# Optimization experiments

Hardware: AMD Instinct MI355X
Metric: run time of the kernel (lower is better)

The kernel has to match this reference:

```python
import jax, jax.numpy as jnp
import numpy as np

N_AUTHOR, N_PAPER = 20000, 40000
E = 400000
IN_DIM, HIDDEN, HEADS, NUM_CLASSES, NUM_LAYERS = 128, 128, 8, 16, 2
DIM = HIDDEN // HEADS
NEG_SLOPE = 0.2
AUTHOR_RAW = 64


def setup_inputs() -> dict:
    key = jax.random.key(0)
    ks = jax.random.split(key, 16)
    s = 0.05
    return {
        'x_author': jax.random.normal(ks[0], (N_AUTHOR, AUTHOR_RAW), jnp.float32),
        'x_paper': jax.random.normal(ks[1], (N_PAPER, IN_DIM), jnp.float32),
        'Wa': jax.random.normal(ks[2], (AUTHOR_RAW, IN_DIM), jnp.float32) * s,
        'proj_w': jax.random.normal(ks[3], (NUM_LAYERS, 2, IN_DIM, HIDDEN), jnp.float32) * s,
        'proj_b': jnp.zeros((NUM_LAYERS, 2, HIDDEN), jnp.float32),
        'att_src': jax.random.normal(ks[4], (NUM_LAYERS, 3, HEADS, DIM), jnp.float32) * s,
        'att_dst': jax.random.normal(ks[5], (NUM_LAYERS, 3, HEADS, DIM), jnp.float32) * s,
        'klin_w': jax.random.normal(ks[6], (NUM_LAYERS, HIDDEN, HIDDEN), jnp.float32) * s,
        'klin_b': jnp.zeros((NUM_LAYERS, HIDDEN), jnp.float32),
        'q': jax.random.normal(ks[7], (NUM_LAYERS, HIDDEN), jnp.float32) * s,
        'lin_w': jax.random.normal(ks[8], (HIDDEN, NUM_CLASSES), jnp.float32) * s,
        'lin_b': jnp.zeros((NUM_CLASSES,), jnp.float32),
        'ei_writes': jnp.stack([jax.random.randint(ks[9], (E,), 0, N_AUTHOR),
                                jax.random.randint(ks[10], (E,), 0, N_PAPER)]),
        'ei_written_by': jnp.stack([jax.random.randint(ks[11], (E,), 0, N_PAPER),
                                    jax.random.randint(ks[12], (E,), 0, N_AUTHOR)]),
        'ei_cites': jnp.stack([jax.random.randint(ks[13], (E,), 0, N_PAPER),
                               jax.random.randint(ks[14], (E,), 0, N_PAPER)]),
    }


def _segment_softmax(scores, seg, num_segments):
    # scores: [E, H]; softmax over edges sharing a destination node.
    m = jax.ops.segment_max(scores, seg, num_segments=num_segments)
    m = jnp.where(jnp.isfinite(m), m, 0.0)
    e = jnp.exp(scores - m[seg])
    denom = jax.ops.segment_sum(e, seg, num_segments=num_segments)
    return e / (denom[seg] + 1e-16)


def _han_forward(x_author, x_paper, Wa, proj_w, proj_b, att_src, att_dst,
                 klin_w, klin_b, q, lin_w, lin_b,
                 ei_writes, ei_written_by, ei_cites):
    # Type-alignment projector (author: 64 -> 128, no bias; paper: Identity)
    x = {'author': x_author @ Wa, 'paper': x_paper}
    nsize = {'author': N_AUTHOR, 'paper': N_PAPER}
    ntidx = {'author': 0, 'paper': 1}
    edge_types = [('author', 'paper', ei_writes),
                  ('paper', 'author', ei_written_by),
                  ('paper', 'paper', ei_cites)]
    for l in range(NUM_LAYERS):
        # Per-node-type projection -> [N, H, D]
        xh = {nt: (x[nt] @ proj_w[l, ntidx[nt]] + proj_b[l, ntidx[nt]]).reshape(-1, HEADS, DIM)
              for nt in x}
        outs = {'author': [], 'paper': []}
        for e_id, (src, dst, ei) in enumerate(edge_types):
            a_src = (xh[src] * att_src[l, e_id]).sum(-1)  # [N_src, H]
            a_dst = (xh[dst] * att_dst[l, e_id]).sum(-1)  # [N_dst, H]
            si, di = ei[0], ei[1]
            alpha = a_src[si] + a_dst[di]                 # [E, H]
            alpha = jnp.where(alpha >= 0, alpha, NEG_SLOPE * alpha)  # leaky_relu
            alpha = _segment_softmax(alpha, di, nsize[dst])
            # attention dropout omitted (eval mode)
            msg = (xh[src][si] * alpha[:, :, None]).reshape(-1, HIDDEN)  # [E, HIDDEN]
            agg = jax.ops.segment_sum(msg, di, num_segments=nsize[dst])
            outs[dst].append(jax.nn.relu(agg))
        # Semantic-level attention over metapath embeddings per node type
        newx = {}
        for nt, xs in outs.items():
            stk = jnp.stack(xs)  # [M, N, F]
            score = (q[l] * jnp.tanh(stk @ klin_w[l] + klin_b[l]).mean(axis=1)).sum(-1)  # [M]
            attn = jax.nn.softmax(score)
            newx[nt] = (attn[:, None, None] * stk).sum(0)
        x = newx
        if l < NUM_LAYERS - 1:
            x = {nt: jax.nn.relu(v) for nt, v in x.items()}
            # feature dropout omitted (eval mode)
    return x['paper'] @ lin_w + lin_b  # [N_PAPER, NUM_CLASSES]


def reference(x_author, x_paper, Wa, proj_w, proj_b, att_src, att_dst,
              klin_w, klin_b, q, lin_w, lin_b,
              ei_writes, ei_written_by, ei_cites):
    return _han_forward(x_author, x_paper, Wa, proj_w, proj_b, att_src, att_dst,
                        klin_w, klin_b, q, lin_w, lin_b,
                        ei_writes, ei_written_by, ei_cites)
```

## Files before the change

### kernel.cpp

```cpp
#include <hip/hip_runtime.h>
#include <hip/hip_bf16.h>

typedef __hip_bfloat16 bf16;
typedef __hip_bfloat162 bf162;

#define N_AUTHOR 20000
#define N_PAPER  40000
#define NEDGE    400000
#define HID      128
#define HEADS    8
#define DIMH     16
#define NCLS     16

typedef short short4v __attribute__((ext_vector_type(4)));
typedef short short8v __attribute__((ext_vector_type(8)));
typedef float f32x4   __attribute__((ext_vector_type(4)));

__device__ __forceinline__ bf162 mk2(float a, float b){
    bf162 r; r.x = __float2bfloat16(a); r.y = __float2bfloat16(b); return r;
}
__device__ __forceinline__ float b2f(short s){
    return __uint_as_float(((unsigned)(unsigned short)s) << 16);
}
__device__ __forceinline__ short f2bs(float v){
    unsigned u = __float_as_uint(v);
    unsigned r = (u + 0x7FFFu + ((u >> 16) & 1u)) >> 16;
    return (short)r;
}
__device__ __forceinline__ float fastrcp(float x){ return __builtin_amdgcn_rcpf(x); }

__device__ __forceinline__ float fast_tanh(float x){
    x = fminf(fmaxf(x, -15.f), 15.f);
    float e = __expf(2.f * x);
    return 1.f - 2.f * fastrcp(e + 1.f);
}

template<int KDIM, int EPI>
__device__ __forceinline__ void bgemm_body(
    const bf16* __restrict__ A, const bf16* __restrict__ Wt, const float* __restrict__ Bb,
    bf16* __restrict__ C, const float* __restrict__ qv, float* __restrict__ score,
    int M, int brow, float* red)
{
    const int tid  = threadIdx.x;
    const int lane = tid & 63;
    const int wv   = tid >> 6;
    const int lr   = lane & 15;
    const int quad = lane >> 4;
    const int row0 = brow * 64 + wv * 16;
    const int arow_i = row0 + lr;
    const bool rowok = arow_i < M;
    const bf16* arow = A + (long)arow_i * KDIM;

    short8v afrag[KDIM / 32];
    #pragma unroll
    for (int kc = 0; kc < KDIM / 32; kc++) {
        short8v f = {0,0,0,0,0,0,0,0};
        if (rowok) f = *(const short8v*)(arow + kc * 32 + quad * 8);
        afrag[kc] = f;
    }

    f32x4 acc[8];
    #pragma unroll
    for (int ct = 0; ct < 8; ct++) acc[ct] = (f32x4){0.f, 0.f, 0.f, 0.f};

    #pragma unroll
    for (int kc = 0; kc < KDIM / 32; kc++) {
        short8v bfrag[8];
        #pragma unroll
        for (int ct = 0; ct < 8; ct++)
            bfrag[ct] = *(const short8v*)(Wt + (long)(ct * 16 + lr) * KDIM + kc * 32 + quad * 8);
        #pragma unroll
        for (int ct = 0; ct < 8; ct++)
            acc[ct] = __builtin_amdgcn_mfma_f32_16x16x32_bf16(afrag[kc], bfrag[ct], acc[ct], 0, 0, 0);
    }

    if (EPI == 0) {
        #pragma unroll
        for (int ct = 0; ct < 8; ct++) {
            float bc = Bb ? Bb[ct * 16 + lr] : 0.f;
            #pragma unroll
            for (int r = 0; r < 4; r++) {
                int orow = row0 + quad * 4 + r;
                if (orow < M)
                    C[(long)orow * HID + ct * 16 + lr] = __float2bfloat16(acc[ct][r] + bc);
            }
        }
    } else {
        float part = 0.f;
        #pragma unroll
        for (int ct = 0; ct < 8; ct++) {
            float bc = Bb ? Bb[ct * 16 + lr] : 0.f;
            float qc = qv[ct * 16 + lr];
            #pragma unroll
            for (int r = 0; r < 4; r++) {
                int orow = row0 + quad * 4 + r;
                if (orow < M) part += qc * fast_tanh(acc[ct][r] + bc);
            }
        }
        red[tid] = part;
        __syncthreads();
        for (int s = 128; s > 0; s >>= 1) {
            if (tid < s) red[tid] += red[tid + s];
            __syncthreads();
        }
        if (tid == 0) atomicAdd(score, red[0]);
    }
}

template<int KDIM, int EPI>
__global__ __launch_bounds__(256) void bgemm_kernel(
    const bf16* __restrict__ A, const bf16* __restrict__ Wt, const float* __restrict__ Bb,
    bf16* __restrict__ C, const float* __restrict__ qv, float* __restrict__ score, int M)
{
    __shared__ float red[256];
    bgemm_body<KDIM, EPI>(A, Wt, Bb, C, qv, score, M, blockIdx.x, red);
}

template<int KDIM, int EPI>
__global__ __launch_bounds__(256) void bgemm_pair_kernel(
    const bf16* __restrict__ A0, const bf16* __restrict__ Wt0, const float* __restrict__ Bb0,
    bf16* __restrict__ C0, float* __restrict__ score0, int M0, int NB0,
    const bf16* __restrict__ A1, const bf16* __restrict__ Wt1, const float* __restrict__ Bb1,
    bf16* __restrict__ C1, float* __restrict__ score1, int M1,
    const float* __restrict__ qv)
{
    __shared__ float red[256];
    const int bx = blockIdx.x;
    if (bx < NB0)
        bgemm_body<KDIM, EPI>(A0, Wt0, Bb0, C0, qv, score0, M0, bx, red);
    else
        bgemm_body<KDIM, EPI>(A1, Wt1, Bb1, C1, qv, score1, M1, bx - NB0, red);
}

#define R_WA  (128 * 64)
#define R_PW  (4 * 128 * 128)
#define R_KW  (2 * 128 * 128)
#define NXA (N_AUTHOR * 64)
#define NXP (N_PAPER * HID)
#define CONV_W_TOT (R_WA + R_PW + R_KW)
#define CONV_X_TOT ((NXA + NXP) / 4)

__global__ void conv_all_kernel(const float* __restrict__ Wa,
                                const float* __restrict__ proj_w,
                                const float* __restrict__ klin_w,
                                const float* __restrict__ xa_f,
                                const float* __restrict__ xp_f,
                                bf16* __restrict__ wt_wa,
                                bf16* __restrict__ wt_proj,
                                bf16* __restrict__ wt_klin,
                                bf16* __restrict__ xa,
                                bf16* __restrict__ xp)
{
    int t = blockIdx.x * blockDim.x + threadIdx.x;
    if (t < CONV_W_TOT) {
        int i = t;
        if (i < R_WA) {
            int n = i >> 6, k = i & 63;
            wt_wa[i] = __float2bfloat16(Wa[k * 128 + n]);
        } else if (i < R_WA + R_PW) {
            int j = i - R_WA;
            int m = j >> 14, r = j & 16383;
            int n = r >> 7, k = r & 127;
            wt_proj[j] = __float2bfloat16(proj_w[m * 16384 + k * 128 + n]);
        } else {
            int j = i - R_WA - R_PW;
            int m = j >> 14, r = j & 16383;
            int n = r >> 7, k = r & 127;
            wt_klin[j] = __float2bfloat16(klin_w[m * 16384 + k * 128 + n]);
        }
    } else if (t < CONV_W_TOT + CONV_X_TOT) {
        int i = (t - CONV_W_TOT) * 4;
        if (i < NXA) {
            float4 v = *(const float4*)(xa_f + i);
            xa[i]   = __float2bfloat16(v.x); xa[i+1] = __float2bfloat16(v.y);
            xa[i+2] = __float2bfloat16(v.z); xa[i+3] = __float2bfloat16(v.w);
        } else {
            int j = i - NXA;
            float4 v = *(const float4*)(xp_f + j);
            xp[j]   = __float2bfloat16(v.x); xp[j+1] = __float2bfloat16(v.y);
            xp[j+2] = __float2bfloat16(v.z); xp[j+3] = __float2bfloat16(v.w);
        }
    }
}

__global__ void node_att_multi_kernel(const bf16* __restrict__ xh,
    const float* __restrict__ A0, const float* __restrict__ A1,
    const float* __restrict__ A2, const float* __restrict__ A3,
    float* __restrict__ O0, float* __restrict__ O1,
    float* __restrict__ O2, float* __restrict__ O3, int N)
{
    int i = blockIdx.x * blockDim.x + threadIdx.x;
    if (i >= N * HEADS) return;
    int n = i >> 3, h = i & 7;
    const bf16* row = xh + (long)n * HID + h * DIMH;
    float x[DIMH];
    #pragma unroll
    for (int d = 0; d < DIMH; d++) x[d] = __bfloat162float(row[d]);
    if (A0) { float s = 0.f;
        #pragma unroll
        for (int d = 0; d < DIMH; d++) s += x[d] * A0[h*DIMH + d];
        O0[i] = s; }
    if (A1) { float s = 0.f;
        #pragma unroll
        for (int d = 0; d < DIMH; d++) s += x[d] * A1[h*DIMH + d];
        O1[i] = s; }
    if (A2) { float s = 0.f;
        #pragma unroll
        for (int d = 0; d < DIMH; d++) s += x[d] * A2[h*DIMH + d];
        O2[i] = s; }
    if (A3) { float s = 0.f;
        #pragma unroll
        for (int d = 0; d < DIMH; d++) s += x[d] * A3[h*DIMH + d];
        O3[i] = s; }
}

#define CNT_OFF1 N_PAPER
#define CNT_OFF2 (N_PAPER + N_AUTHOR)
#define E3 (3 * NEDGE)
#define HIST_T (E3 / 4)

__global__ void hist3_kernel(const int* __restrict__ d0, const int* __restrict__ d1,
                             const int* __restrict__ d2, int* __restrict__ cnt,
                             unsigned short* __restrict__ rank)
{
    int t = blockIdx.x * blockDim.x + threadIdx.x;
    if (t >= HIST_T) return;
    #pragma unroll
    for (int u = 0; u < 4; u++) {
        int i = t + u * HIST_T;
        int r;
        if (i < NEDGE)            r = atomicAdd(&cnt[d0[i]], 1);
        else if (i < 2*NEDGE)     r = atomicAdd(&cnt[CNT_OFF1 + d1[i - NEDGE]], 1);
        else                      r = atomicAdd(&cnt[CNT_OFF2 + d2[i - 2*NEDGE]], 1);
        rank[i] = (unsigned short)r;
    }
}

__device__ __forceinline__ int job_nd(int j){ return j == 1 ? N_AUTHOR : N_PAPER; }
__device__ __forceinline__ int job_off(int j){ return j == 0 ? 0 : (j == 1 ? CNT_OFF1 : CNT_OFF2); }

__global__ __launch_bounds__(256) void scan_a3_kernel(const int* __restrict__ cnt,
                                                      int* __restrict__ bsum)
{
    int j = blockIdx.y;
    int nd = job_nd(j), off = job_off(j);
    __shared__ int s[256];
    int tid = threadIdx.x;
    int i = blockIdx.x * 256 + tid;
    s[tid] = (i < nd) ? cnt[off + i] : 0;
    __syncthreads();
    for (int st = 128; st > 0; st >>= 1) {
        if (tid < st) s[tid] += s[tid + st];
        __syncthreads();
    }
    if (tid == 0) bsum[j * 256 + blockIdx.x] = s[0];
}

__global__ __launch_bounds__(256) void scan_b3_kernel(int* __restrict__ bsum,
    int* __restrict__ roff0, int* __restrict__ roff1, int* __restrict__ roff2)
{
    int j = blockIdx.x;
    int nd = job_nd(j);
    int nb = (nd + 255) / 256;
    int* roff = j == 0 ? roff0 : (j == 1 ? roff1 : roff2);
    __shared__ int s[256];
    int tid = threadIdx.x;
    int v = (tid < nb) ? bsum[j * 256 + tid] : 0;
    s[tid] = v;
    __syncthreads();
    for (int off = 1; off < 256; off <<= 1) {
        int t = (tid >= off) ? s[tid - off] : 0;
        __syncthreads();
        s[tid] += t;
        __syncthreads();
    }
    if (tid < nb) bsum[j * 256 + tid] = s[tid] - v;
    if (tid == 255) roff[nd] = s[255];
}

__global__ __launch_bounds__(256) void scan_c3_kernel(const int* __restrict__ cnt,
    const int* __restrict__ bsum,
    int* __restrict__ roff0, int* __restrict__ roff1, int* __restrict__ roff2)
{
    int j = blockIdx.y;
    int nd = job_nd(j), off = job_off(j);
    int* roff = j == 0 ? roff0 : (j == 1 ? roff1 : roff2);
    __shared__ int s[256];
    int tid = threadIdx.x;
    int i = blockIdx.x * 256 + tid;
    int v = (i < nd) ? cnt[off + i] : 0;
    s[tid] = v;
    __syncthreads();
    for (int o = 1; o < 256; o <<= 1) {
        int t = (tid >= o) ? s[tid - o] : 0;
        __syncthreads();
        s[tid] += t;
        __syncthreads();
    }
    if (i < nd) roff[i] = bsum[j * 256 + blockIdx.x] + s[tid] - v;
}

__global__ void fill3_kernel(
    const int* __restrict__ s0, const int* __restrict__ d0,
    const int* __restrict__ s1, const int* __restrict__ d1,
    const int* __restrict__ s2, const int* __restrict__ d2,
    const int* __restrict__ roff0, const int* __restrict__ roff1, const int* __restrict__ roff2,
    const unsigned short* __restrict__ rank,
    unsigned short* __restrict__ c0, unsigned short* __restrict__ c1, unsigned short* __restrict__ c2)
{
    int t = blockIdx.x * blockDim.x + threadIdx.x;
    if (t >= HIST_T) return;
    #pragma unroll
    for (int u = 0; u < 4; u++) {
        int i = t + u * HIST_T;
        if (i < NEDGE) {
            int d = d0[i];
            c0[roff0[d] + rank[i]] = (unsigned short)s0[i];
        } else if (i < 2*NEDGE) {
            int e = i - NEDGE, d = d1[e];
            c1[roff1[d] + rank[i]] = (unsigned short)s1[e];
        } else {
            int e = i - 2*NEDGE, d = d2[e];
            c2[roff2[d] + rank[i]] = (unsigned short)s2[e];
        }
    }
}

__global__ __launch_bounds__(256) void paper_gather2_kernel(
    const int* __restrict__ roff0, const unsigned short* __restrict__ csrc0,
    const float* __restrict__ as0, const float* __restrict__ ad0,
    const bf16* __restrict__ xha,
    const int* __restrict__ roff2, const unsigned short* __restrict__ csrc2,
    const float* __restrict__ as2, const float* __restrict__ ad2,
    const bf16* __restrict__ xhp,
    bf16* __restrict__ out0, bf16* __restrict__ out2)
{
    int lane = threadIdx.x & 63;
    int li   = lane & 15;
    int sub  = lane >> 4;
    int w = blockIdx.x * 16 + (threadIdx.x >> 6) * 4 + sub;
    if (w >= N_PAPER) return;
    int h = li >> 1;

    int b0 = roff0[w], n0 = roff0[w + 1] - b0;
    int b2 = roff2[w], n2 = roff2[w + 1] - b2;
    float ad0v = ad0[(long)w * 8 + h];
    float ad2v = ad2[(long)w * 8 + h];
    float den0 = 0.f, den2 = 0.f;
    float acc0[8], acc2[8];
    #pragma unroll
    for (int j = 0; j < 8; j++) { acc0[j] = 0.f; acc2[j] = 0.f; }

    int nmax = n0 > n2 ? n0 : n2;
    int c0m = n0 > 0 ? n0 - 1 : 0;
    int c2m = n2 > 0 ? n2 - 1 : 0;
    for (int i = 0; i < nmax; i += 4) {
        int sA[4], sB[4];
        #pragma unroll
        for (int u = 0; u < 4; u++) {
            sA[u] = csrc0[b0 + min(i + u, c0m)];
            sB[u] = csrc2[b2 + min(i + u, c2m)];
        }
        float aA[4], aB[4];
        short8v xA[4], xB[4];
        #pragma unroll
        for (int u = 0; u < 4; u++) {
            aA[u] = as0[(long)sA[u] * 8 + h];
            xA[u] = *(const short8v*)(xha + (long)sA[u] * HID + li * 8);
            aB[u] = as2[(long)sB[u] * 8 + h];
            xB[u] = *(const short8v*)(xhp + (long)sB[u] * HID + li * 8);
        }
        #pragma unroll
        for (int u = 0; u < 4; u++) {
            float a = aA[u] + ad0v;
            a = a >= 0.f ? a : 0.2f * a;
            float wt = __expf(fminf(a, 60.f));
            wt = (i + u < n0) ? wt : 0.f;
            den0 += wt;
            #pragma unroll
            for (int j = 0; j < 8; j++)
                acc0[j] = fmaf(b2f(xA[u][j]), wt, acc0[j]);
            a = aB[u] + ad2v;
            a = a >= 0.f ? a : 0.2f * a;
            wt = __expf(fminf(a, 60.f));
            wt = (i + u < n2) ? wt : 0.f;
            den2 += wt;
            #pragma unroll
            for (int j = 0; j < 8; j++)
                acc2[j] = fmaf(b2f(xB[u][j]), wt, acc2[j]);
        }
    }
    float inv0 = fastrcp(den0 + 1e-16f);
    float inv2 = fastrcp(den2 + 1e-16f);
    short8v o0, o2;
    #pragma unroll
    for (int j = 0; j < 8; j++) {
        o0[j] = f2bs(fmaxf(acc0[j] * inv0, 0.f));
        o2[j] = f2bs(fmaxf(acc2[j] * inv2, 0.f));
    }
    *(short8v*)(out0 + (long)w * HID + li * 8) = o0;
    *(short8v*)(out2 + (long)w * HID + li * 8) = o2;
}

__global__ __launch_bounds__(256) void edge_gather_kernel(
    const int* __restrict__ roff, const unsigned short* __restrict__ csrc,
    const float* __restrict__ as_, const float* __restrict__ ad_,
    const bf16* __restrict__ xh, bf16* __restrict__ out, int Ndst)
{
    int lane = threadIdx.x & 63;
    int li   = lane & 15;
    int sub  = lane >> 4;
    int w = blockIdx.x * 16 + (threadIdx.x >> 6) * 4 + sub;
    if (w >= Ndst) return;
    int h = li >> 1;
    int beg = roff[w], n = roff[w + 1] - beg;
    float adv = ad_[(long)w * 8 + h];
    float den = 0.f;
    float acc[8];
    #pragma unroll
    for (int j = 0; j < 8; j++) acc[j] = 0.f;
    int cm = n > 0 ? n - 1 : 0;
    for (int i = 0; i < n; i += 4) {
        int s[4];
        #pragma unroll
        for (int u = 0; u < 4; u++) s[u] = csrc[beg + min(i + u, cm)];
        float av[4]; short8v xv[4];
        #pragma unroll
        for (int u = 0; u < 4; u++) {
            av[u] = as_[(long)s[u] * 8 + h];
            xv[u] = *(const short8v*)(xh + (long)s[u] * HID + li * 8);
        }
        #pragma unroll
        for (int u = 0; u < 4; u++) {
            float a = av[u] + adv;
            a = a >= 0.f ? a : 0.2f * a;
            float wt = __expf(fminf(a, 60.f));
            wt = (i + u < n) ? wt : 0.f;
            den += wt;
            #pragma unroll
            for (int j = 0; j < 8; j++)
                acc[j] = fmaf(b2f(xv[u][j]), wt, acc[j]);
        }
    }
    float inv = fastrcp(den + 1e-16f);
    short8v o;
    #pragma unroll
    for (int j = 0; j < 8; j++) o[j] = f2bs(fmaxf(acc[j] * inv, 0.f));
    *(short8v*)(out + (long)w * HID + li * 8) = o;
}

__global__ void combine_kernel(const bf16* __restrict__ a0, const bf16* __restrict__ a1,
                               const float* __restrict__ score, bf16* __restrict__ out, int n2)
{
    int i = blockIdx.x * blockDim.x + threadIdx.x;
    if (i >= n2) return;
    float s0 = score[0] * (1.f / N_PAPER);
    float s1 = score[1] * (1.f / N_PAPER);
    float m = fmaxf(s0, s1);
    float e0 = __expf(s0 - m), e1 = __expf(s1 - m);
    float inv = fastrcp(e0 + e1);
    float w0 = e0 * inv, w1 = e1 * inv;
    bf162 v0 = ((const bf162*)a0)[i];
    bf162 v1 = ((const bf162*)a1)[i];
    ((bf162*)out)[i] = mk2(w0 * __bfloat162float(v0.x) + w1 * __bfloat162float(v1.x),
                           w0 * __bfloat162float(v0.y) + w1 * __bfloat162float(v1.y));
}

__global__ __launch_bounds__(256) void final_lin_fused_kernel(
    const bf16* __restrict__ a0, const bf16* __restrict__ a1,
    const float* __restrict__ score,
    const float* __restrict__ W, const float* __restrict__ B, float* __restrict__ out)
{
    __shared__ float Ws[HID * NCLS];
    int tid = threadIdx.x;
    for (int i = tid; i < HID * NCLS; i += 256) Ws[i] = W[i];
    __syncthreads();
    float s0 = score[0] * (1.f / N_PAPER);
    float s1 = score[1] * (1.f / N_PAPER);
    float m = fmaxf(s0, s1);
    float e0 = __expf(s0 - m), e1 = __expf(s1 - m);
    float inv = 1.f / (e0 + e1);
    float w0 = e0 * inv, w1 = e1 * inv;
    int i = blockIdx.x * 256 + tid;
    if (i >= N_PAPER * NCLS) return;
    int n = i >> 4, c = i & 15;
    float acc = B[c];
    const bf16* x0 = a0 + (long)n * HID;
    const bf16* x1 = a1 + (long)n * HID;
    #pragma unroll 16
    for (int k = 0; k < HID; k++)
        acc = fmaf(fmaf(w0, __bfloat162float(x0[k]), w1 * __bfloat162float(x1[k])),
                   Ws[k * NCLS + c], acc);
    out[i] = acc;
}

extern "C" void kernel_launch(void* const* d_in, const int* in_sizes, int n_in,
                              void* d_out, int out_size, void* d_ws, size_t ws_size,
                              hipStream_t stream)
{
    const float* x_author = (const float*)d_in[0];
    const float* x_paper  = (const float*)d_in[1];
    const float* Wa       = (const float*)d_in[2];
    const float* proj_w   = (const float*)d_in[3];
    const float* proj_b   = (const float*)d_in[4];
    const float* att_src  = (const float*)d_in[5];
    const float* att_dst  = (const float*)d_in[6];
    const float* klin_w   = (const float*)d_in[7];
    const float* klin_b   = (const float*)d_in[8];
    const float* qv       = (const float*)d_in[9];
    const float* lin_w    = (const float*)d_in[10];
    const float* lin_b    = (const float*)d_in[11];
    const int*  ei_w      = (const int*)d_in[12];
    const int*  ei_wb     = (const int*)d_in[13];
    const int*  ei_c      = (const int*)d_in[14];
    float* out = (float*)d_out;
    (void)ws_size; (void)in_sizes; (void)n_in; (void)out_size;

    char* base = (char*)d_ws;
    size_t off = 0;
    auto alloc = [&](size_t bytes) {
        void* p = base + off;
        off = (off + bytes + 255) & ~(size_t)255;
        return p;
    };
    bf16*  xh_a  = (bf16*) alloc((size_t)N_AUTHOR * HID * 2);
    bf16*  xh_p  = (bf16*) alloc((size_t)N_PAPER  * HID * 2);
    bf16*  buf_a = (bf16*) alloc((size_t)N_AUTHOR * HID * 2);
    bf16*  buf_p = (bf16*) alloc((size_t)N_PAPER  * HID * 2);
    bf16*  agg_p1= (bf16*) alloc((size_t)N_PAPER  * HID * 2);
    bf16*  xa    = (bf16*) alloc((size_t)N_AUTHOR * 64  * 2);
    bf16*  xp    = (bf16*) alloc((size_t)N_PAPER  * HID * 2);
    bf16*  wt_wa   = (bf16*)alloc((size_t)R_WA * 2);
    bf16*  wt_proj = (bf16*)alloc((size_t)R_PW * 2);
    bf16*  wt_klin = (bf16*)alloc((size_t)R_KW * 2);
    float* a_e0s = (float*)alloc((size_t)N_AUTHOR * HEADS * 4);
    float* a_e0d = (float*)alloc((size_t)N_PAPER  * HEADS * 4);
    float* a_e1s = (float*)alloc((size_t)N_PAPER  * HEADS * 4);
    float* a_e1d = (float*)alloc((size_t)N_AUTHOR * HEADS * 4);
    float* a_e2s = (float*)alloc((size_t)N_PAPER  * HEADS * 4);
    float* a_e2d = (float*)alloc((size_t)N_PAPER  * HEADS * 4);
    float* score  = (float*)alloc(64);
    int* roff0 = (int*)alloc((size_t)(N_PAPER  + 1) * 4);
    int* roff1 = (int*)alloc((size_t)(N_AUTHOR + 1) * 4);
    int* roff2 = (int*)alloc((size_t)(N_PAPER  + 1) * 4);
    unsigned short* csrc0 = (unsigned short*)alloc((size_t)NEDGE * 2 + 64);
    unsigned short* csrc1 = (unsigned short*)alloc((size_t)NEDGE * 2 + 64);
    unsigned short* csrc2 = (unsigned short*)alloc((size_t)NEDGE * 2 + 64);
    int* cnt   = (int*)alloc((size_t)(2 * N_PAPER + N_AUTHOR) * 4);
    unsigned short* rank = (unsigned short*)alloc((size_t)E3 * 2);
    int* bsum  = (int*)alloc(3 * 256 * 4);

    const int GA = (N_AUTHOR + 63) / 64;
    const int GP = (N_PAPER  + 63) / 64;
    const int NBMAX = (N_PAPER + 255) / 256;

    conv_all_kernel<<<(CONV_W_TOT + CONV_X_TOT + 255)/256, 256, 0, stream>>>(
        Wa, proj_w, klin_w, x_author, x_paper,
        wt_wa, wt_proj, wt_klin, xa, xp);

    hipMemsetAsync(cnt, 0, (size_t)(2 * N_PAPER + N_AUTHOR) * 4, stream);
    hist3_kernel<<<(HIST_T + 255)/256, 256, 0, stream>>>(
        ei_w + NEDGE, ei_wb + NEDGE, ei_c + NEDGE, cnt, rank);
    scan_a3_kernel<<<dim3(NBMAX, 3), 256, 0, stream>>>(cnt, bsum);
    scan_b3_kernel<<<3, 256, 0, stream>>>(bsum, roff0, roff1, roff2);
    scan_c3_kernel<<<dim3(NBMAX, 3), 256, 0, stream>>>(cnt, bsum, roff0, roff1, roff2);
    fill3_kernel<<<(HIST_T + 255)/256, 256, 0, stream>>>(
        ei_w, ei_w + NEDGE, ei_wb, ei_wb + NEDGE, ei_c, ei_c + NEDGE,
        roff0, roff1, roff2, rank, csrc0, csrc1, csrc2);

    bgemm_kernel<64, 0><<<GA, 256, 0, stream>>>(
        xa, wt_wa, nullptr, buf_a, nullptr, nullptr, N_AUTHOR);

    for (int l = 0; l < 2; l++) {
        const bool last = (l == 1);
        const bf16* cur_a = buf_a;
        const bf16* cur_p = (l == 0) ? xp : buf_p;
        const bf16* pw_a = wt_proj + (size_t)(l*2 + 0) * HID * HID;
        const bf16* pw_p = wt_proj + (size_t)(l*2 + 1) * HID * HID;
        const float* pb_a = proj_b + (size_t)(l*2 + 0) * HID;
        const float* pb_p = proj_b + (size_t)(l*2 + 1) * HID;

        bgemm_pair_kernel<128, 0><<<GA + GP, 256, 0, stream>>>(
            cur_a, pw_a, pb_a, xh_a, nullptr, N_AUTHOR, GA,
            cur_p, pw_p, pb_p, xh_p, nullptr, N_PAPER, nullptr);

        hipMemsetAsync(score, 0, 64, stream);

        const float* as0 = att_src + (size_t)(l*3 + 0) * HID;
        const float* ad0 = att_dst + (size_t)(l*3 + 0) * HID;
        const float* as1 = att_src + (size_t)(l*3 + 1) * HID;
        const float* ad1 = att_dst + (size_t)(l*3 + 1) * HID;
        const float* as2 = att_src + (size_t)(l*3 + 2) * HID;
        const float* ad2 = att_dst + (size_t)(l*3 + 2) * HID;

        node_att_multi_kernel<<<(N_AUTHOR*HEADS + 255)/256, 256, 0, stream>>>(
            xh_a, as0, last ? nullptr : ad1, nullptr, nullptr,
            a_e0s, a_e1d, nullptr, nullptr, N_AUTHOR);
        node_att_multi_kernel<<<(N_PAPER*HEADS + 255)/256, 256, 0, stream>>>(
            xh_p, ad0, last ? nullptr : as1, as2, ad2,
            a_e0d, a_e1s, a_e2s, a_e2d, N_PAPER);

        paper_gather2_kernel<<<(N_PAPER + 15)/16, 256, 0, stream>>>(
            roff0, csrc0, a_e0s, a_e0d, xh_a,
            roff2, csrc2, a_e2s, a_e2d, xh_p,
            buf_p, agg_p1);
        if (!last)
            edge_gather_kernel<<<(N_AUTHOR + 15)/16, 256, 0, stream>>>(
                roff1, csrc1, a_e1s, a_e1d, xh_p, buf_a, N_AUTHOR);

        const bf16* kw = wt_klin + (size_t)l * HID * HID;
        const float* kb = klin_b + (size_t)l * HID;
        const float* qq = qv     + (size_t)l * HID;
        bgemm_pair_kernel<128, 1><<<2 * GP, 256, 0, stream>>>(
            buf_p, kw, kb, (bf16*)nullptr, score + 0, N_PAPER, GP,
            agg_p1, kw, kb, (bf16*)nullptr, score + 1, N_PAPER, qq);

        if (!last)
            combine_kernel<<<(N_PAPER*HID/2 + 255)/256, 256, 0, stream>>>(
                buf_p, agg_p1, score, buf_p, N_PAPER*HID/2);
    }

    final_lin_fused_kernel<<<(N_PAPER*NCLS + 255)/256, 256, 0, stream>>>(
        buf_p, agg_p1, score, lin_w, lin_b, out);
}
```

Baseline: 455.1 us.

## Fuse histogram with conversion and CSR fill with author GEMM; pad counters

Merges the edge-count histogram kernel into the weight/feature conversion kernel and the CSR fill kernel into the author input GEMM kernel, dispatching by block index. This removes two kernel launches and lets independent work overlap on the GPU. The counter array is padded to a stride of 16 ints so that atomics on different destinations fall on separate cache lines. The GEMM inner loop now loads B fragments for two K-chunks before issuing MFMAs, which raises register use. The padding adds memset and scan-read traffic on a larger counter buffer.

After: 444.6 us. 1.02x faster.

```diff
diff --git a/kernel.cpp b/kernel.cpp
--- a/kernel.cpp
+++ b/kernel.cpp
@@ -64,14 +64,18 @@
     for (int ct = 0; ct < 8; ct++) acc[ct] = (f32x4){0.f, 0.f, 0.f, 0.f};
 
     #pragma unroll
-    for (int kc = 0; kc < KDIM / 32; kc++) {
-        short8v bfrag[8];
-        #pragma unroll
-        for (int ct = 0; ct < 8; ct++)
-            bfrag[ct] = *(const short8v*)(Wt + (long)(ct * 16 + lr) * KDIM + kc * 32 + quad * 8);
-        #pragma unroll
-        for (int ct = 0; ct < 8; ct++)
-            acc[ct] = __builtin_amdgcn_mfma_f32_16x16x32_bf16(afrag[kc], bfrag[ct], acc[ct], 0, 0, 0);
+    for (int k0 = 0; k0 < KDIM / 32; k0 += 2) {
+        short8v bf[2][8];
+        #pragma unroll
+        for (int u = 0; u < 2; u++)
+            #pragma unroll
+            for (int ct = 0; ct < 8; ct++)
+                bf[u][ct] = *(const short8v*)(Wt + (long)(ct * 16 + lr) * KDIM + (k0 + u) * 32 + quad * 8);
+        #pragma unroll
+        for (int u = 0; u < 2; u++)
+            #pragma unroll
+            for (int ct = 0; ct < 8; ct++)
+                acc[ct] = __builtin_amdgcn_mfma_f32_16x16x32_bf16(afrag[k0 + u], bf[u][ct], acc[ct], 0, 0, 0);
     }
 
     if (EPI == 0) {
@@ -108,15 +112,6 @@
 }
 
 template<int KDIM, int EPI>
-__global__ __launch_bounds__(256) void bgemm_kernel(
-    const bf16* __restrict__ A, const bf16* __restrict__ Wt, const float* __restrict__ Bb,
-    bf16* __restrict__ C, const float* __restrict__ qv, float* __restrict__ score, int M)
-{
-    __shared__ float red[256];
-    bgemm_body<KDIM, EPI>(A, Wt, Bb, C, qv, score, M, blockIdx.x, red);
-}
-
-template<int KDIM, int EPI>
 __global__ __launch_bounds__(256) void bgemm_pair_kernel(
     const bf16* __restrict__ A0, const bf16* __restrict__ Wt0, const float* __restrict__ Bb0,
     bf16* __restrict__ C0, float* __restrict__ score0, int M0, int NB0,
@@ -139,19 +134,40 @@
 #define NXP (N_PAPER * HID)
 #define CONV_W_TOT (R_WA + R_PW + R_KW)
 #define CONV_X_TOT ((NXA + NXP) / 4)
-
-__global__ void conv_all_kernel(const float* __restrict__ Wa,
-                                const float* __restrict__ proj_w,
-                                const float* __restrict__ klin_w,
-                                const float* __restrict__ xa_f,
-                                const float* __restrict__ xp_f,
-                                bf16* __restrict__ wt_wa,
-                                bf16* __restrict__ wt_proj,
-                                bf16* __restrict__ wt_klin,
-                                bf16* __restrict__ xa,
-                                bf16* __restrict__ xp)
-{
-    int t = blockIdx.x * blockDim.x + threadIdx.x;
+#define CONV_TOT   (CONV_W_TOT + CONV_X_TOT)
+
+#define CNT_OFF1 N_PAPER
+#define CNT_OFF2 (N_PAPER + N_AUTHOR)
+#define NDEST    (2 * N_PAPER + N_AUTHOR)
+#define CSTR     16
+#define E3 (3 * NEDGE)
+#define HIST_T (E3 / 4)
+
+__global__ __launch_bounds__(256) void conv_hist_kernel(
+    const int* __restrict__ d0, const int* __restrict__ d1, const int* __restrict__ d2,
+    int* __restrict__ cnt, unsigned short* __restrict__ rank, int HB,
+    const float* __restrict__ Wa, const float* __restrict__ proj_w,
+    const float* __restrict__ klin_w,
+    const float* __restrict__ xa_f, const float* __restrict__ xp_f,
+    bf16* __restrict__ wt_wa, bf16* __restrict__ wt_proj, bf16* __restrict__ wt_klin,
+    bf16* __restrict__ xa, bf16* __restrict__ xp)
+{
+    int bx = blockIdx.x;
+    if (bx < HB) {
+        int t = bx * 256 + threadIdx.x;
+        if (t >= HIST_T) return;
+        #pragma unroll
+        for (int u = 0; u < 4; u++) {
+            int i = t + u * HIST_T;
+            int r;
+            if (i < NEDGE)            r = atomicAdd(&cnt[(long)d0[i] * CSTR], 1);
+            else if (i < 2*NEDGE)     r = atomicAdd(&cnt[(long)(CNT_OFF1 + d1[i - NEDGE]) * CSTR], 1);
+            else                      r = atomicAdd(&cnt[(long)(CNT_OFF2 + d2[i - 2*NEDGE]) * CSTR], 1);
+            rank[i] = (unsigned short)r;
+        }
+        return;
+    }
+    int t = (bx - HB) * 256 + threadIdx.x;
     if (t < CONV_W_TOT) {
         int i = t;
         if (i < R_WA) {
@@ -168,7 +184,7 @@
             int n = r >> 7, k = r & 127;
             wt_klin[j] = __float2bfloat16(klin_w[m * 16384 + k * 128 + n]);
         }
-    } else if (t < CONV_W_TOT + CONV_X_TOT) {
+    } else if (t < CONV_TOT) {
         int i = (t - CONV_W_TOT) * 4;
         if (i < NXA) {
             float4 v = *(const float4*)(xa_f + i);
@@ -183,59 +199,6 @@
     }
 }
 
-__global__ void node_att_multi_kernel(const bf16* __restrict__ xh,
-    const float* __restrict__ A0, const float* __restrict__ A1,
-    const float* __restrict__ A2, const float* __restrict__ A3,
-    float* __restrict__ O0, float* __restrict__ O1,
-    float* __restrict__ O2, float* __restrict__ O3, int N)
-{
-    int i = blockIdx.x * blockDim.x + threadIdx.x;
-    if (i >= N * HEADS) return;
-    int n = i >> 3, h = i & 7;
-    const bf16* row = xh + (long)n * HID + h * DIMH;
-    float x[DIMH];
-    #pragma unroll
-    for (int d = 0; d < DIMH; d++) x[d] = __bfloat162float(row[d]);
-    if (A0) { float s = 0.f;
-        #pragma unroll
-        for (int d = 0; d < DIMH; d++) s += x[d] * A0[h*DIMH + d];
-        O0[i] = s; }
-    if (A1) { float s = 0.f;
-        #pragma unroll
-        for (int d = 0; d < DIMH; d++) s += x[d] * A1[h*DIMH + d];
-        O1[i] = s; }
-    if (A2) { float s = 0.f;
-        #pragma unroll
-        for (int d = 0; d < DIMH; d++) s += x[d] * A2[h*DIMH + d];
-        O2[i] = s; }
-    if (A3) { float s = 0.f;
-        #pragma unroll
-        for (int d = 0; d < DIMH; d++) s += x[d] * A3[h*DIMH + d];
-        O3[i] = s; }
-}
-
-#define CNT_OFF1 N_PAPER
-#define CNT_OFF2 (N_PAPER + N_AUTHOR)
-#define E3 (3 * NEDGE)
-#define HIST_T (E3 / 4)
-
-__global__ void hist3_kernel(const int* __restrict__ d0, const int* __restrict__ d1,
-                             const int* __restrict__ d2, int* __restrict__ cnt,
-                             unsigned short* __restrict__ rank)
-{
-    int t = blockIdx.x * blockDim.x + threadIdx.x;
-    if (t >= HIST_T) return;
-    #pragma unroll
-    for (int u = 0; u < 4; u++) {
-        int i = t + u * HIST_T;
-        int r;
-        if (i < NEDGE)            r = atomicAdd(&cnt[d0[i]], 1);
-        else if (i < 2*NEDGE)     r = atomicAdd(&cnt[CNT_OFF1 + d1[i - NEDGE]], 1);
-        else                      r = atomicAdd(&cnt[CNT_OFF2 + d2[i - 2*NEDGE]], 1);
-        rank[i] = (unsigned short)r;
-    }
-}
-
 __device__ __forceinline__ int job_nd(int j){ return j == 1 ? N_AUTHOR : N_PAPER; }
 __device__ __forceinline__ int job_off(int j){ return j == 0 ? 0 : (j == 1 ? CNT_OFF1 : CNT_OFF2); }
 
@@ -247,7 +210,7 @@
     __shared__ int s[256];
     int tid = threadIdx.x;
     int i = blockIdx.x * 256 + tid;
-    s[tid] = (i < nd) ? cnt[off + i] : 0;
+    s[tid] = (i < nd) ? cnt[(long)(off + i) * CSTR] : 0;
     __syncthreads();
     for (int st = 128; st > 0; st >>= 1) {
         if (tid < st) s[tid] += s[tid + st];
@@ -288,7 +251,7 @@
     __shared__ int s[256];
     int tid = threadIdx.x;
     int i = blockIdx.x * 256 + tid;
-    int v = (i < nd) ? cnt[off + i] : 0;
+    int v = (i < nd) ? cnt[(long)(off + i) * CSTR] : 0;
     s[tid] = v;
     __syncthreads();
     for (int o = 1; o < 256; o <<= 1) {
@@ -300,7 +263,9 @@
     if (i < nd) roff[i] = bsum[j * 256 + blockIdx.x] + s[tid] - v;
 }
 
-__global__ void fill3_kernel(
+__global__ __launch_bounds__(256) void fill_gemm_kernel(
+    const bf16* __restrict__ A, const bf16* __restrict__ Wt, bf16* __restrict__ C,
+    int M, int GAb,
     const int* __restrict__ s0, const int* __restrict__ d0,
     const int* __restrict__ s1, const int* __restrict__ d1,
     const int* __restrict__ s2, const int* __restrict__ d2,
@@ -308,7 +273,13 @@
     const unsigned short* __restrict__ rank,
     unsigned short* __restrict__ c0, unsigned short* __restrict__ c1, unsigned short* __restrict__ c2)
 {
-    int t = blockIdx.x * blockDim.x + threadIdx.x;
+    __shared__ float red[256];
+    int bx = blockIdx.x;
+    if (bx < GAb) {
+        bgemm_body<64, 0>(A, Wt, nullptr, C, nullptr, nullptr, M, bx, red);
+        return;
+    }
+    int t = (bx - GAb) * 256 + threadIdx.x;
     if (t >= HIST_T) return;
     #pragma unroll
     for (int u = 0; u < 4; u++) {
@@ -324,6 +295,37 @@
             c2[roff2[d] + rank[i]] = (unsigned short)s2[e];
         }
     }
+}
+
+__global__ void node_att_multi_kernel(const bf16* __restrict__ xh,
+    const float* __restrict__ A0, const float* __restrict__ A1,
+    const float* __restrict__ A2, const float* __restrict__ A3,
+    float* __restrict__ O0, float* __restrict__ O1,
+    float* __restrict__ O2, float* __restrict__ O3, int N)
+{
+    int i = blockIdx.x * blockDim.x + threadIdx.x;
+    if (i >= N * HEADS) return;
+    int n = i >> 3, h = i & 7;
+    const bf16* row = xh + (long)n * HID + h * DIMH;
+    float x[DIMH];
+    #pragma unroll
+    for (int d = 0; d < DIMH; d++) x[d] = __bfloat162float(row[d]);
+    if (A0) { float s = 0.f;
+        #pragma unroll
+        for (int d = 0; d < DIMH; d++) s += x[d] * A0[h*DIMH + d];
+        O0[i] = s; }
+    if (A1) { float s = 0.f;
+        #pragma unroll
+        for (int d = 0; d < DIMH; d++) s += x[d] * A1[h*DIMH + d];
+        O1[i] = s; }
+    if (A2) { float s = 0.f;
+        #pragma unroll
+        for (int d = 0; d < DIMH; d++) s += x[d] * A2[h*DIMH + d];
+        O2[i] = s; }
+    if (A3) { float s = 0.f;
+        #pragma unroll
+        for (int d = 0; d < DIMH; d++) s += x[d] * A3[h*DIMH + d];
+        O3[i] = s; }
 }
 
 __global__ __launch_bounds__(256) void paper_gather2_kernel(
@@ -546,30 +548,28 @@
     unsigned short* csrc0 = (unsigned short*)alloc((size_t)NEDGE * 2 + 64);
     unsigned short* csrc1 = (unsigned short*)alloc((size_t)NEDGE * 2 + 64);
     unsigned short* csrc2 = (unsigned short*)alloc((size_t)NEDGE * 2 + 64);
-    int* cnt   = (int*)alloc((size_t)(2 * N_PAPER + N_AUTHOR) * 4);
+    int* cnt   = (int*)alloc((size_t)NDEST * CSTR * 4);
     unsigned short* rank = (unsigned short*)alloc((size_t)E3 * 2);
     int* bsum  = (int*)alloc(3 * 256 * 4);
 
     const int GA = (N_AUTHOR + 63) / 64;
     const int GP = (N_PAPER  + 63) / 64;
     const int NBMAX = (N_PAPER + 255) / 256;
-
-    conv_all_kernel<<<(CONV_W_TOT + CONV_X_TOT + 255)/256, 256, 0, stream>>>(
+    const int HB = (HIST_T + 255) / 256;
+    const int CONVB = (CONV_TOT + 255) / 256;
+
+    hipMemsetAsync(cnt, 0, (size_t)NDEST * CSTR * 4, stream);
+    conv_hist_kernel<<<HB + CONVB, 256, 0, stream>>>(
+        ei_w + NEDGE, ei_wb + NEDGE, ei_c + NEDGE, cnt, rank, HB,
         Wa, proj_w, klin_w, x_author, x_paper,
         wt_wa, wt_proj, wt_klin, xa, xp);
-
-    hipMemsetAsync(cnt, 0, (size_t)(2 * N_PAPER + N_AUTHOR) * 4, stream);
-    hist3_kernel<<<(HIST_T + 255)/256, 256, 0, stream>>>(
-        ei_w + NEDGE, ei_wb + NEDGE, ei_c + NEDGE, cnt, rank);
     scan_a3_kernel<<<dim3(NBMAX, 3), 256, 0, stream>>>(cnt, bsum);
     scan_b3_kernel<<<3, 256, 0, stream>>>(bsum, roff0, roff1, roff2);
     scan_c3_kernel<<<dim3(NBMAX, 3), 256, 0, stream>>>(cnt, bsum, roff0, roff1, roff2);
-    fill3_kernel<<<(HIST_T + 255)/256, 256, 0, stream>>>(
+    fill_gemm_kernel<<<GA + HB, 256, 0, stream>>>(
+        xa, wt_wa, buf_a, N_AUTHOR, GA,
         ei_w, ei_w + NEDGE, ei_wb, ei_wb + NEDGE, ei_c, ei_c + NEDGE,
         roff0, roff1, roff2, rank, csrc0, csrc1, csrc2);
-
-    bgemm_kernel<64, 0><<<GA, 256, 0, stream>>>(
-        xa, wt_wa, nullptr, buf_a, nullptr, nullptr, N_AUTHOR);
 
     for (int l = 0; l < 2; l++) {
         const bool last = (l == 1);
```
